# Kernel tuning notes

Hardware: AMD Instinct MI355X
Metric: run time of the kernel (lower is better)

The kernel has to match this reference:

```python
import jax, jax.numpy as jnp
from jax import lax
import numpy as np

NEG_SLOPE = 0.01  # PyTorch LeakyReLU default


def setup_inputs() -> dict:
    key = jax.random.key(0)
    ks = jax.random.split(key, 7)
    B, Ns, T, C = 32, 512, 128, 25
    proj_dim, H = 20, 25
    s_lin = 1.0 / np.sqrt(C)
    s_gru = 1.0 / np.sqrt(H)
    return {
        "x": jax.random.normal(ks[0], (B, Ns, T, C), jnp.float32),
        "W1": jax.random.uniform(ks[1], (proj_dim, C), jnp.float32, -s_lin, s_lin),
        "b1": jax.random.uniform(ks[2], (proj_dim,), jnp.float32, -s_lin, s_lin),
        "W_ih": jax.random.uniform(ks[3], (3 * H, proj_dim), jnp.float32, -s_gru, s_gru),
        "W_hh": jax.random.uniform(ks[4], (3 * H, H), jnp.float32, -s_gru, s_gru),
        "b_ih": jax.random.uniform(ks[5], (3 * H,), jnp.float32, -s_gru, s_gru),
        "b_hh": jax.random.uniform(ks[6], (3 * H,), jnp.float32, -s_gru, s_gru),
    }


def reference(x, W1, b1, W_ih, W_hh, b_ih, b_hh):
    # Linear + LeakyReLU projection: [B, Ns, T, 25] -> [B, Ns, T, proj_dim]
    p = jnp.einsum("bntc,pc->bntp", x, W1) + b1
    p = jnp.where(p >= 0, p, NEG_SLOPE * p)

    B, Ns, T, P = p.shape
    H = W_hh.shape[1]
    p = p.reshape(B * Ns, T, P)

    # Precompute input-side gate pre-activations for all timesteps: [N, T, 3H]
    gx = jnp.einsum("ntp,gp->ntg", p, W_ih) + b_ih
    gx = jnp.swapaxes(gx, 0, 1)  # [T, N, 3H] for scan

    def step(h, gx_t):
        gh = h @ W_hh.T + b_hh  # [N, 3H]
        xr, xz, xn = jnp.split(gx_t, 3, axis=-1)
        hr, hz, hn = jnp.split(gh, 3, axis=-1)
        r = jax.nn.sigmoid(xr + hr)
        z = jax.nn.sigmoid(xz + hz)
        n = jnp.tanh(xn + r * hn)
        h_new = (1.0 - z) * n + z * h
        return h_new, None

    h0 = jnp.zeros((B * Ns, H), p.dtype)
    hT, _ = lax.scan(step, h0, gx)
    return hT.reshape(B, Ns, H)
```

## Files before the change

### kernel.cpp

```cpp
#include <hip/hip_runtime.h>


typedef __bf16 bf16x8 __attribute__((ext_vector_type(8)));
typedef float  f32x4  __attribute__((ext_vector_type(4)));

#define TT 128
#define CC 25
#define PP 20
#define HH 25
#define NSEQ 16384
#define S  36
#define MFMA __builtin_amdgcn_mfma_f32_16x16x32_bf16
#define LD_ACQ(p)    __hip_atomic_load((p), __ATOMIC_ACQUIRE, __HIP_MEMORY_SCOPE_WORKGROUP)
#define ST_REL(p, v) __hip_atomic_store((p), (v), __ATOMIC_RELEASE, __HIP_MEMORY_SCOPE_WORKGROUP)

__device__ __forceinline__ void split2(float f, __bf16& hi, __bf16& lo) {
    hi = (__bf16)f;
    lo = (__bf16)(f - (float)hi);
}
__device__ __forceinline__ float frcp(float v) { return __builtin_amdgcn_rcpf(v); }

__global__ __launch_bounds__(128, 2) void gru_ring(
    const float* __restrict__ x,   const float* __restrict__ W1,
    const float* __restrict__ b1,  const float* __restrict__ Wih,
    const float* __restrict__ Whh, const float* __restrict__ bih,
    const float* __restrict__ bhh, float* __restrict__ out)
{
    __shared__ float sp[16 * S];
    __shared__ float sh[2][16 * S];
    __shared__ f32x4 sgx[4][64][6];
    __shared__ int s_prod, s_cons;

    const int tid  = threadIdx.x;
    const bool pw  = (tid < 64);
    const int lane = tid & 63;
    const int m = lane & 15, q = lane >> 4;
    const int n0 = blockIdx.x * 16;

    for (int idx = tid; idx < 16 * S; idx += 128) {
        sp[idx] = 0.f; sh[0][idx] = 0.f; sh[1][idx] = 0.f;
    }
    if (tid == 0) { s_prod = 0; s_cons = 0; }
    __syncthreads();
    if (tid < 16) {
        sp[tid * S + PP]    = 1.0f;
        sh[0][tid * S + HH] = 1.0f;
        sh[1][tid * S + HH] = 1.0f;
    }
    __syncthreads();

    bf16x8 WgH[6], WgL[6], WpH[2], WpL[2];
    {
        const float* Ws = pw ? Wih : Whh;
        const float* bs = pw ? bih : bhh;
        const int kd    = pw ? PP  : HH;
        #pragma unroll
        for (int tt = 0; tt < 6; ++tt) {
            const int g = tt >> 1;
            const int u = (tt & 1) * 16 + m;
            const bool uv = (u < HH);
            const int row = g * HH + u;
            bf16x8 h8, l8;
            #pragma unroll
            for (int j = 0; j < 8; ++j) {
                const int k = q * 8 + j;
                float v = 0.f;
                if (uv) {
                    if (k < kd)       v = Ws[row * kd + k];
                    else if (k == kd) v = bs[row];
                }
                __bf16 a, b; split2(v, a, b); h8[j] = a; l8[j] = b;
            }
            WgH[tt] = h8; WgL[tt] = l8;
        }
    }
    if (pw) {
        #pragma unroll
        for (int tt = 0; tt < 2; ++tt) {
            const int u = tt * 16 + m;
            const bool uv = (u < PP);
            bf16x8 h8, l8;
            #pragma unroll
            for (int j = 0; j < 8; ++j) {
                const int k = q * 8 + j;
                float v = 0.f;
                if (uv) {
                    if (k < CC)       v = W1[u * CC + k];
                    else if (k == CC) v = b1[u];
                }
                __bf16 a, b; split2(v, a, b); h8[j] = a; l8[j] = b;
            }
            WpH[tt] = h8; WpL[tt] = l8;
        }
    }

    if (pw) {
        const float* xrow = x + (size_t)(n0 + m) * (TT * CC);
        const int cbase = (q < 3) ? q * 8 : 21;
        float xc[8];

        auto load_x = [&](int t) {
            const float* xr = xrow + t * CC;
            f32x4 va = *(const f32x4*)(xr + cbase);
            f32x4 vb = *(const f32x4*)(xr + cbase + ((q < 3) ? 4 : 0));
            #pragma unroll
            for (int j = 0; j < 8; ++j) {
                float v;
                if (q < 3) v = (j < 4) ? va[j] : vb[j - 4];
                else       v = (j == 0) ? va[3] : (j == 1 ? 1.0f : 0.0f);
                xc[j] = v;
            }
        };

        auto produce = [&](int tc, int slot) {
            bf16x8 xH, xL;
            #pragma unroll
            for (int j = 0; j < 8; ++j) { __bf16 a,b; split2(xc[j],a,b); xH[j]=a; xL[j]=b; }

            {
                const int tn = (tc + 1 < TT) ? tc + 1 : TT - 1;
                load_x(tn);
            }

            f32x4 p0 = {0.f,0.f,0.f,0.f}, p1 = {0.f,0.f,0.f,0.f};
            p0 = MFMA(WpH[0], xH, p0, 0,0,0);
            p0 = MFMA(WpH[0], xL, p0, 0,0,0);
            p0 = MFMA(WpL[0], xH, p0, 0,0,0);
            p1 = MFMA(WpH[1], xH, p1, 0,0,0);
            p1 = MFMA(WpH[1], xL, p1, 0,0,0);
            p1 = MFMA(WpL[1], xH, p1, 0,0,0);
            #pragma unroll
            for (int r = 0; r < 4; ++r) {
                p0[r] = (p0[r] >= 0.f) ? p0[r] : 0.01f * p0[r];
                p1[r] = (p1[r] >= 0.f) ? p1[r] : 0.01f * p1[r];
            }

            *(f32x4*)(sp + m * S + 4 * q) = p0;
            if (q == 0) *(f32x4*)(sp + m * S + 16) = p1;

            f32x4 pa = ((const f32x4*)(sp + m * S + 8 * q))[0];
            f32x4 pb = ((const f32x4*)(sp + m * S + 8 * q))[1];
            bf16x8 pH, pL;
            #pragma unroll
            for (int j = 0; j < 4; ++j) {
                __bf16 a, b;
                split2(pa[j], a, b); pH[j]   = a; pL[j]   = b;
                split2(pb[j], a, b); pH[4+j] = a; pL[4+j] = b;
            }

            f32x4* ring = &sgx[slot][lane][0];
            #pragma unroll
            for (int tp = 0; tp < 2; ++tp) {
                f32x4 acc = {0.f,0.f,0.f,0.f};
                acc = MFMA(WgH[tp], pH, acc, 0,0,0);
                acc = MFMA(WgH[tp], pL, acc, 0,0,0);
                acc = MFMA(WgL[tp], pH, acc, 0,0,0);
                ring[tp] = acc;
                f32x4 az = {0.f,0.f,0.f,0.f};
                az = MFMA(WgH[2+tp], pH, az, 0,0,0);
                az = MFMA(WgH[2+tp], pL, az, 0,0,0);
                az = MFMA(WgL[2+tp], pH, az, 0,0,0);
                ring[2+tp] = az;
                f32x4 an = {0.f,0.f,0.f,0.f};
                an = MFMA(WgH[4+tp], pH, an, 0,0,0);
                an = MFMA(WgH[4+tp], pL, an, 0,0,0);
                an = MFMA(WgL[4+tp], pH, an, 0,0,0);
                ring[4+tp] = an;
            }
        };

        load_x(0);
        int known_cons = 0;
        for (int tb = 0; tb < TT; tb += 4) {
            #pragma unroll
            for (int u = 0; u < 4; ++u) {
                const int t = tb + u;
                if (t >= 4 && known_cons < t - 3) {
                    do { known_cons = LD_ACQ(&s_cons); } while (known_cons < t - 3);
                }
                produce(t, u);
                if (lane == 0) ST_REL(&s_prod, t + 1);
            }
        }
    } else {
        float ho[2][4] = {{0.f,0.f,0.f,0.f},{0.f,0.f,0.f,0.f}};
        int known_prod = 0;

        auto consume = [&](int t, int slot) {
            const int par = slot & 1;
            const float* hrow = sh[par] + m * S + 8 * q;
            f32x4 ha = ((const f32x4*)hrow)[0];
            f32x4 hb = ((const f32x4*)hrow)[1];
            bf16x8 hH, hL;
            #pragma unroll
            for (int j = 0; j < 4; ++j) {
                __bf16 a, b;
                split2(ha[j], a, b); hH[j]   = a; hL[j]   = b;
                split2(hb[j], a, b); hH[4+j] = a; hL[4+j] = b;
            }
            const f32x4* ring = &sgx[slot][lane][0];
            f32x4 aR[2], aZ[2], aHn[2], gN[2];
            #pragma unroll
            for (int tp = 0; tp < 2; ++tp) {
                f32x4 acc = ring[tp];
                acc = MFMA(WgH[tp], hH, acc, 0,0,0);
                acc = MFMA(WgH[tp], hL, acc, 0,0,0);
                acc = MFMA(WgL[tp], hH, acc, 0,0,0);
                aR[tp] = acc;
                f32x4 az = ring[2+tp];
                az = MFMA(WgH[2+tp], hH, az, 0,0,0);
                az = MFMA(WgH[2+tp], hL, az, 0,0,0);
                az = MFMA(WgL[2+tp], hH, az, 0,0,0);
                aZ[tp] = az;
                gN[tp] = ring[4+tp];
                f32x4 ah = {0.f,0.f,0.f,0.f};
                ah = MFMA(WgH[4+tp], hH, ah, 0,0,0);
                ah = MFMA(WgH[4+tp], hL, ah, 0,0,0);
                ah = MFMA(WgL[4+tp], hH, ah, 0,0,0);
                aHn[tp] = ah;
            }
            #pragma unroll
            for (int tp = 0; tp < 2; ++tp) {
                f32x4 hv;
                #pragma unroll
                for (int r = 0; r < 4; ++r) {
                    const float rg = frcp(1.f + __expf(-aR[tp][r]));
                    const float zg = frcp(1.f + __expf(-aZ[tp][r]));
                    const float nv = gN[tp][r] + rg * aHn[tp][r];
                    const float e  = __expf(-2.f * nv);
                    const float ng = 2.f * frcp(1.f + e) - 1.f;
                    const float h2 = zg * (ho[tp][r] - ng) + ng;
                    ho[tp][r] = h2; hv[r] = h2;
                }
                float* dst = sh[par ^ 1] + m * S + tp * 16 + 4 * q;
                if (tp == 0) {
                    *(f32x4*)dst = hv;
                } else {
                    if (q < 2)       *(f32x4*)dst = hv;
                    else if (q == 2) dst[0] = hv[0];
                }
            }
        };

        for (int tb = 0; tb < TT; tb += 4) {
            #pragma unroll
            for (int u = 0; u < 4; ++u) {
                const int t = tb + u;
                if (known_prod < t + 1) {
                    do { known_prod = LD_ACQ(&s_prod); } while (known_prod < t + 1);
                }
                consume(t, u);
                if (lane == 0) ST_REL(&s_cons, t + 1);
            }
        }

        float* orow = out + (size_t)(n0 + m) * HH;
        #pragma unroll
        for (int tp = 0; tp < 2; ++tp) {
            #pragma unroll
            for (int r = 0; r < 4; ++r) {
                const int u = tp * 16 + 4 * q + r;
                if (u < HH) orow[u] = ho[tp][r];
            }
        }
    }
}

extern "C" void kernel_launch(void* const* d_in, const int* in_sizes, int n_in,
                              void* d_out, int out_size, void* d_ws, size_t ws_size,
                              hipStream_t stream) {
    const float* x   = (const float*)d_in[0];
    const float* W1  = (const float*)d_in[1];
    const float* b1  = (const float*)d_in[2];
    const float* Wih = (const float*)d_in[3];
    const float* Whh = (const float*)d_in[4];
    const float* bih = (const float*)d_in[5];
    const float* bhh = (const float*)d_in[6];
    float* out = (float*)d_out;

    gru_ring<<<NSEQ / 16, 128, 0, stream>>>(x, W1, b1, Wih, Whh, bih, bhh, out);
}
```

Before: 358.5 us.

## Split GRU recurrence across two consumer wavefronts with pairwise step handshake

Each block now runs three wavefronts: one producer computes the projection and input gates, and two consumers each own one 16-unit tile of the hidden state. Each consumer computes its own r/z/n gates, and the two sync every step through per-consumer counters so the double-buffered hidden state stays consistent. The gate ring layout is changed to [slot][tile][lane] so each consumer reads a contiguous slice. This halves the serial MFMA and transcendental chain per step on the critical path. In exchange it adds an extra cross-wave spin-wait each step and more wavefronts per block, which may lower occupancy.

```diff
diff --git a/kernel.cpp b/kernel.cpp
--- a/kernel.cpp
+++ b/kernel.cpp
@@ -20,7 +20,7 @@
 }
 __device__ __forceinline__ float frcp(float v) { return __builtin_amdgcn_rcpf(v); }
 
-__global__ __launch_bounds__(128, 2) void gru_ring(
+__global__ __launch_bounds__(192, 3) void gru_3w(
     const float* __restrict__ x,   const float* __restrict__ W1,
     const float* __restrict__ b1,  const float* __restrict__ Wih,
     const float* __restrict__ Whh, const float* __restrict__ bih,
@@ -28,19 +28,19 @@
 {
     __shared__ float sp[16 * S];
     __shared__ float sh[2][16 * S];
-    __shared__ f32x4 sgx[4][64][6];
-    __shared__ int s_prod, s_cons;
+    __shared__ f32x4 sgx[4][6][64];
+    __shared__ int s_prod, s_c0, s_c1;
 
     const int tid  = threadIdx.x;
-    const bool pw  = (tid < 64);
+    const int wid  = tid >> 6;
     const int lane = tid & 63;
     const int m = lane & 15, q = lane >> 4;
     const int n0 = blockIdx.x * 16;
 
-    for (int idx = tid; idx < 16 * S; idx += 128) {
+    for (int idx = tid; idx < 16 * S; idx += 192) {
         sp[idx] = 0.f; sh[0][idx] = 0.f; sh[1][idx] = 0.f;
     }
-    if (tid == 0) { s_prod = 0; s_cons = 0; }
+    if (tid == 0) { s_prod = 0; s_c0 = 0; s_c1 = 0; }
     __syncthreads();
     if (tid < 16) {
         sp[tid * S + PP]    = 1.0f;
@@ -49,11 +49,8 @@
     }
     __syncthreads();
 
-    bf16x8 WgH[6], WgL[6], WpH[2], WpL[2];
-    {
-        const float* Ws = pw ? Wih : Whh;
-        const float* bs = pw ? bih : bhh;
-        const int kd    = pw ? PP  : HH;
+    if (wid == 0) {
+        bf16x8 WgH[6], WgL[6], WpH[2], WpL[2];
         #pragma unroll
         for (int tt = 0; tt < 6; ++tt) {
             const int g = tt >> 1;
@@ -66,15 +63,13 @@
                 const int k = q * 8 + j;
                 float v = 0.f;
                 if (uv) {
-                    if (k < kd)       v = Ws[row * kd + k];
-                    else if (k == kd) v = bs[row];
+                    if (k < PP)       v = Wih[row * PP + k];
+                    else if (k == PP) v = bih[row];
                 }
                 __bf16 a, b; split2(v, a, b); h8[j] = a; l8[j] = b;
             }
             WgH[tt] = h8; WgL[tt] = l8;
         }
-    }
-    if (pw) {
         #pragma unroll
         for (int tt = 0; tt < 2; ++tt) {
             const int u = tt * 16 + m;
@@ -92,9 +87,7 @@
             }
             WpH[tt] = h8; WpL[tt] = l8;
         }
-    }
-
-    if (pw) {
+
         const float* xrow = x + (size_t)(n0 + m) * (TT * CC);
         const int cbase = (q < 3) ? q * 8 : 21;
         float xc[8];
@@ -148,120 +141,132 @@
                 split2(pb[j], a, b); pH[4+j] = a; pL[4+j] = b;
             }
 
-            f32x4* ring = &sgx[slot][lane][0];
+            f32x4* ring = &sgx[slot][0][lane];
             #pragma unroll
             for (int tp = 0; tp < 2; ++tp) {
                 f32x4 acc = {0.f,0.f,0.f,0.f};
                 acc = MFMA(WgH[tp], pH, acc, 0,0,0);
                 acc = MFMA(WgH[tp], pL, acc, 0,0,0);
                 acc = MFMA(WgL[tp], pH, acc, 0,0,0);
-                ring[tp] = acc;
+                ring[(0 + tp) * 64] = acc;
                 f32x4 az = {0.f,0.f,0.f,0.f};
                 az = MFMA(WgH[2+tp], pH, az, 0,0,0);
                 az = MFMA(WgH[2+tp], pL, az, 0,0,0);
                 az = MFMA(WgL[2+tp], pH, az, 0,0,0);
-                ring[2+tp] = az;
+                ring[(2 + tp) * 64] = az;
                 f32x4 an = {0.f,0.f,0.f,0.f};
                 an = MFMA(WgH[4+tp], pH, an, 0,0,0);
                 an = MFMA(WgH[4+tp], pL, an, 0,0,0);
                 an = MFMA(WgL[4+tp], pH, an, 0,0,0);
-                ring[4+tp] = an;
+                ring[(4 + tp) * 64] = an;
             }
         };
 
         load_x(0);
-        int known_cons = 0;
+        int kc0 = 0, kc1 = 0;
         for (int tb = 0; tb < TT; tb += 4) {
             #pragma unroll
-            for (int u = 0; u < 4; ++u) {
-                const int t = tb + u;
-                if (t >= 4 && known_cons < t - 3) {
-                    do { known_cons = LD_ACQ(&s_cons); } while (known_cons < t - 3);
-                }
-                produce(t, u);
+            for (int u4 = 0; u4 < 4; ++u4) {
+                const int t = tb + u4;
+                if (t >= 4) {
+                    if (kc0 < t - 3) do { kc0 = LD_ACQ(&s_c0); } while (kc0 < t - 3);
+                    if (kc1 < t - 3) do { kc1 = LD_ACQ(&s_c1); } while (kc1 < t - 3);
+                }
+                produce(t, u4);
                 if (lane == 0) ST_REL(&s_prod, t + 1);
             }
         }
     } else {
-        float ho[2][4] = {{0.f,0.f,0.f,0.f},{0.f,0.f,0.f,0.f}};
-        int known_prod = 0;
-
-        auto consume = [&](int t, int slot) {
-            const int par = slot & 1;
-            const float* hrow = sh[par] + m * S + 8 * q;
-            f32x4 ha = ((const f32x4*)hrow)[0];
-            f32x4 hb = ((const f32x4*)hrow)[1];
-            bf16x8 hH, hL;
-            #pragma unroll
-            for (int j = 0; j < 4; ++j) {
-                __bf16 a, b;
-                split2(ha[j], a, b); hH[j]   = a; hL[j]   = b;
-                split2(hb[j], a, b); hH[4+j] = a; hL[4+j] = b;
-            }
-            const f32x4* ring = &sgx[slot][lane][0];
-            f32x4 aR[2], aZ[2], aHn[2], gN[2];
-            #pragma unroll
-            for (int tp = 0; tp < 2; ++tp) {
-                f32x4 acc = ring[tp];
-                acc = MFMA(WgH[tp], hH, acc, 0,0,0);
-                acc = MFMA(WgH[tp], hL, acc, 0,0,0);
-                acc = MFMA(WgL[tp], hH, acc, 0,0,0);
-                aR[tp] = acc;
-                f32x4 az = ring[2+tp];
-                az = MFMA(WgH[2+tp], hH, az, 0,0,0);
-                az = MFMA(WgH[2+tp], hL, az, 0,0,0);
-                az = MFMA(WgL[2+tp], hH, az, 0,0,0);
-                aZ[tp] = az;
-                gN[tp] = ring[4+tp];
-                f32x4 ah = {0.f,0.f,0.f,0.f};
-                ah = MFMA(WgH[4+tp], hH, ah, 0,0,0);
-                ah = MFMA(WgH[4+tp], hL, ah, 0,0,0);
-                ah = MFMA(WgL[4+tp], hH, ah, 0,0,0);
-                aHn[tp] = ah;
-            }
-            #pragma unroll
-            for (int tp = 0; tp < 2; ++tp) {
+        const bool c0 = (wid == 1);
+        const int ctp = wid - 1;
+        bf16x8 WrH, WrL, WzH, WzL, WnH, WnL;
+        {
+            const int u = ctp * 16 + m;
+            const bool uv = (u < HH);
+            #pragma unroll
+            for (int g = 0; g < 3; ++g) {
+                const int row = g * HH + u;
+                bf16x8 h8, l8;
+                #pragma unroll
+                for (int j = 0; j < 8; ++j) {
+                    const int k = q * 8 + j;
+                    float v = 0.f;
+                    if (uv) {
+                        if (k < HH)       v = Whh[row * HH + k];
+                        else if (k == HH) v = bhh[row];
+                    }
+                    __bf16 a, b; split2(v, a, b); h8[j] = a; l8[j] = b;
+                }
+                if (g == 0)      { WrH = h8; WrL = l8; }
+                else if (g == 1) { WzH = h8; WzL = l8; }
+                else             { WnH = h8; WnL = l8; }
+            }
+        }
+
+        float ho[4] = {0.f, 0.f, 0.f, 0.f};
+        int* other = c0 ? &s_c1 : &s_c0;
+        int* own   = c0 ? &s_c0 : &s_c1;
+        int kp = 0, ko = 0;
+
+        for (int tb = 0; tb < TT; tb += 4) {
+            #pragma unroll
+            for (int u4 = 0; u4 < 4; ++u4) {
+                const int t = tb + u4;
+                if (kp < t + 1) do { kp = LD_ACQ(&s_prod); } while (kp < t + 1);
+                if (ko < t)     do { ko = LD_ACQ(other);   } while (ko < t);
+
+                const float* hrow = sh[u4 & 1] + m * S + 8 * q;
+                f32x4 ha = ((const f32x4*)hrow)[0];
+                f32x4 hb = ((const f32x4*)hrow)[1];
+                bf16x8 hH, hL;
+                #pragma unroll
+                for (int j = 0; j < 4; ++j) {
+                    __bf16 a, b;
+                    split2(ha[j], a, b); hH[j]   = a; hL[j]   = b;
+                    split2(hb[j], a, b); hH[4+j] = a; hL[4+j] = b;
+                }
+                const f32x4* rc = &sgx[u4][ctp][lane];
+                f32x4 aRv = rc[0];
+                aRv = MFMA(WrH, hH, aRv, 0,0,0);
+                aRv = MFMA(WrH, hL, aRv, 0,0,0);
+                aRv = MFMA(WrL, hH, aRv, 0,0,0);
+                f32x4 aZv = rc[128];
+                aZv = MFMA(WzH, hH, aZv, 0,0,0);
+                aZv = MFMA(WzH, hL, aZv, 0,0,0);
+                aZv = MFMA(WzL, hH, aZv, 0,0,0);
+                f32x4 gNv = rc[256];
+                f32x4 aHv = {0.f,0.f,0.f,0.f};
+                aHv = MFMA(WnH, hH, aHv, 0,0,0);
+                aHv = MFMA(WnH, hL, aHv, 0,0,0);
+                aHv = MFMA(WnL, hH, aHv, 0,0,0);
+
                 f32x4 hv;
                 #pragma unroll
                 for (int r = 0; r < 4; ++r) {
-                    const float rg = frcp(1.f + __expf(-aR[tp][r]));
-                    const float zg = frcp(1.f + __expf(-aZ[tp][r]));
-                    const float nv = gN[tp][r] + rg * aHn[tp][r];
+                    const float rg = frcp(1.f + __expf(-aRv[r]));
+                    const float zg = frcp(1.f + __expf(-aZv[r]));
+                    const float nv = gNv[r] + rg * aHv[r];
                     const float e  = __expf(-2.f * nv);
                     const float ng = 2.f * frcp(1.f + e) - 1.f;
-                    const float h2 = zg * (ho[tp][r] - ng) + ng;
-                    ho[tp][r] = h2; hv[r] = h2;
-                }
-                float* dst = sh[par ^ 1] + m * S + tp * 16 + 4 * q;
-                if (tp == 0) {
+                    const float h2 = zg * (ho[r] - ng) + ng;
+                    ho[r] = h2; hv[r] = h2;
+                }
+                float* dst = sh[(u4 & 1) ^ 1] + m * S + ctp * 16 + 4 * q;
+                if (c0) {
                     *(f32x4*)dst = hv;
                 } else {
                     if (q < 2)       *(f32x4*)dst = hv;
                     else if (q == 2) dst[0] = hv[0];
                 }
-            }
-        };
-
-        for (int tb = 0; tb < TT; tb += 4) {
-            #pragma unroll
-            for (int u = 0; u < 4; ++u) {
-                const int t = tb + u;
-                if (known_prod < t + 1) {
-                    do { known_prod = LD_ACQ(&s_prod); } while (known_prod < t + 1);
-                }
-                consume(t, u);
-                if (lane == 0) ST_REL(&s_cons, t + 1);
+                if (lane == 0) ST_REL(own, t + 1);
             }
         }
 
         float* orow = out + (size_t)(n0 + m) * HH;
         #pragma unroll
-        for (int tp = 0; tp < 2; ++tp) {
-            #pragma unroll
-            for (int r = 0; r < 4; ++r) {
-                const int u = tp * 16 + 4 * q + r;
-                if (u < HH) orow[u] = ho[tp][r];
-            }
+        for (int r = 0; r < 4; ++r) {
+            const int u = ctp * 16 + 4 * q + r;
+            if (u < HH) orow[u] = ho[r];
         }
     }
 }
@@ -278,5 +283,5 @@
     const float* bhh = (const float*)d_in[6];
     float* out = (float*)d_out;
 
-    gru_ring<<<NSEQ / 16, 128, 0, stream>>>(x, W1, b1, Wih, Whh, bih, bhh, out);
+    gru_3w<<<NSEQ / 16, 192, 0, stream>>>(x, W1, b1, Wih, Whh, bih, bhh, out);
 }
```

Result: slower. 386.9 us (+7.9%).
